# Kernel tuning notes

Measured on AMD Instinct MI355X. Metric: run time of the kernel, lower is better.

The kernel has to match this reference:

```python
import jax, jax.numpy as jnp
import numpy as np

WS = 8        # window_size
NH = 16       # num_heads

def setup_inputs() -> dict:
    key = jax.random.key(0)
    ks = jax.random.split(key, 6)
    B, H, W, C = 16, 64, 64, 512
    nW = (H // WS) * (W // WS)
    return {
        "x": jax.random.normal(ks[0], (B, H * W, C), jnp.float32),
        "qkv_w": jax.random.normal(ks[1], (3 * C, C), jnp.float32) * 0.02,
        "qkv_b": jax.random.normal(ks[2], (3 * C,), jnp.float32) * 0.02,
        "proj_w": jax.random.normal(ks[3], (C, C), jnp.float32) * 0.02,
        "proj_b": jax.random.normal(ks[4], (C,), jnp.float32) * 0.02,
        "attn_mask": jax.random.normal(ks[5], (nW, WS * WS, WS * WS), jnp.float32),
        "H": H,
        "W": W,
    }

def reference(x, qkv_w, qkv_b, proj_w, proj_b, attn_mask, H, W):
    B, N, C = x.shape
    ws = WS
    hd = C // NH
    scale = hd ** (-0.5)
    x_img = x.reshape(B, H, W, C)
    pad_h = (ws - H % ws) % ws
    pad_w = (ws - W % ws) % ws
    if pad_h > 0 or pad_w > 0:
        x_img = jnp.pad(x_img, ((0, 0), (0, pad_h), (0, pad_w), (0, 0)))
    Hp, Wp = H + pad_h, W + pad_w
    nW = (Hp // ws) * (Wp // ws)
    # window partition: [B*nW, ws*ws, C]
    x_win = x_img.reshape(B, Hp // ws, ws, Wp // ws, ws, C)
    x_win = x_win.transpose(0, 1, 3, 2, 4, 5).reshape(B * nW, ws * ws, C)
    # fused qkv projection (torch Linear: y = x @ W^T + b)
    qkv = x_win @ qkv_w.T + qkv_b
    qkv = qkv.reshape(B * nW, ws * ws, 3, NH, hd).transpose(2, 0, 3, 1, 4)
    q, k, v = qkv[0], qkv[1], qkv[2]  # each [B*nW, NH, ws*ws, hd]
    attn = jnp.einsum('bhqd,bhkd->bhqk', q, k) * scale
    if attn_mask is not None:
        attn = attn.reshape(B, nW, NH, ws * ws, ws * ws)
        attn = attn + attn_mask[None, :, None, :, :]
        attn = attn.reshape(B * nW, NH, ws * ws, ws * ws)
    attn = jax.nn.softmax(attn, axis=-1)
    out = jnp.einsum('bhqk,bhkd->bhqd', attn, v)
    out = out.transpose(0, 2, 1, 3).reshape(B * nW, ws * ws, C)
    out = out @ proj_w.T + proj_b
    # window reverse
    out = out.reshape(B, Hp // ws, Wp // ws, ws, ws, C)
    out = out.transpose(0, 1, 3, 2, 4, 5).reshape(B, Hp, Wp, C)
    out = out[:, :H, :W, :].reshape(B, H * W, C)
    return out
```

## Files before the change

kernel.cpp:

```cpp
#include <hip/hip_runtime.h>


typedef unsigned short u16;
typedef unsigned int u32;
typedef __attribute__((ext_vector_type(4))) u16 u16x4;
typedef __attribute__((ext_vector_type(8))) u16 u16x8;
typedef __attribute__((ext_vector_type(8))) short short8;
typedef __attribute__((ext_vector_type(4))) float f32x4;

__device__ __forceinline__ u16 f2bf(float f) {
    u32 u = __float_as_uint(f);
    u += 0x7fffu + ((u >> 16) & 1u);
    return (u16)(u >> 16);
}

__device__ __forceinline__ f32x4 MFMA(u16x8 a, u16x8 b, f32x4 c) {
    return __builtin_amdgcn_mfma_f32_16x16x32_bf16(
        __builtin_bit_cast(short8, a), __builtin_bit_cast(short8, b), c, 0, 0, 0);
}

__device__ __forceinline__ void gload16(const void* g, void* l) {
    __builtin_amdgcn_global_load_lds(
        (const __attribute__((address_space(1))) void*)g,
        (__attribute__((address_space(3))) void*)l, 16, 0, 0);
}

__device__ __forceinline__ int win2img(int r) {
    int b = r >> 12;
    int w = (r >> 6) & 63;
    int t = r & 63;
    int img = (((w >> 3) << 3) + (t >> 3)) * 64 + ((w & 7) << 3) + (t & 7);
    return (b << 12) + img;
}

__device__ __forceinline__ u16x8 cvt8(const float* src) {
    float4 a = *(const float4*)src;
    float4 b = *(const float4*)(src + 4);
    u16x8 t;
    t[0] = f2bf(a.x); t[1] = f2bf(a.y); t[2] = f2bf(a.z); t[3] = f2bf(a.w);
    t[4] = f2bf(b.x); t[5] = f2bf(b.y); t[6] = f2bf(b.z); t[7] = f2bf(b.w);
    return t;
}

__global__ __launch_bounds__(256)
void conv_f2b(const float* __restrict__ in, u16* __restrict__ out, int n8) {
    int u = blockIdx.x * 256 + threadIdx.x;
    if (u >= n8) return;
    *(u16x8*)(out + (size_t)u * 8) = cvt8(in + (size_t)u * 8);
}

__global__ __launch_bounds__(256)
void conv_permute_x(const float* __restrict__ x, u16* __restrict__ xw) {
    int u = blockIdx.x * 256 + threadIdx.x;
    int r = u >> 6;
    int c = (u & 63) << 3;
    int g = win2img(r);
    *(u16x8*)(xw + (size_t)r * 512 + c) = cvt8(x + (size_t)g * 512 + c);
}

__global__ __launch_bounds__(256)
void conv_maskT(const float* __restrict__ mask, float* __restrict__ mT) {
    __shared__ float t[64][65];
    const int w = blockIdx.x;
    const float* mp = mask + ((size_t)w << 12);
    float* op = mT + ((size_t)w << 12);
    const int r = threadIdx.x >> 2, c0 = (threadIdx.x & 3) << 4;
#pragma unroll
    for (int i = 0; i < 4; ++i) {
        float4 v = *(const float4*)(mp + (r << 6) + c0 + i * 4);
        t[c0 + i * 4 + 0][r] = v.x;
        t[c0 + i * 4 + 1][r] = v.y;
        t[c0 + i * 4 + 2][r] = v.z;
        t[c0 + i * 4 + 3][r] = v.w;
    }
    __syncthreads();
#pragma unroll
    for (int i = 0; i < 4; ++i) {
        float4 v;
        v.x = t[r][c0 + i * 4 + 0];
        v.y = t[r][c0 + i * 4 + 1];
        v.z = t[r][c0 + i * 4 + 2];
        v.w = t[r][c0 + i * 4 + 3];
        *(float4*)(op + (r << 6) + c0 + i * 4) = v;
    }
}

__global__ __launch_bounds__(256, 4)
void gemm_qkv(const u16* __restrict__ A, const u16* __restrict__ Wt,
              const float* __restrict__ bias, u16* __restrict__ QK,
              u16* __restrict__ VT)
{
    __shared__ char lds[32768];

    const int nwg = gridDim.x;
    const int q   = nwg >> 3;
    const int wg  = ((int)blockIdx.x & 7) * q + ((int)blockIdx.x >> 3);
    const int m0  = (wg / 12) * 128;
    const int n0  = (wg % 12) * 128;

    const int tid  = threadIdx.x;
    const int lane = tid & 63;
    const int wv   = tid >> 6;
    const int wm   = (wv >> 1) << 6;
    const int wn   = (wv & 1) << 6;
    const int lr   = lane & 15;
    const int lg   = lane >> 4;

    const char* aptr = (const char*)A + (((size_t)(m0 + (tid >> 2))) << 10) + ((tid & 3) << 4);
    const char* bptr = (const char*)Wt + (((size_t)(n0 + (tid >> 2))) << 10) + ((tid & 3) << 4);
    const u32 tb = (u32)tid << 4;

    f32x4 acc[4][4] = {};

#define STAGE(buf, kt) do {                                                   \
    const int ko_ = (kt) * 64;                                                \
    char* d_ = lds + (buf) * 16384 + tb;                                      \
    gload16(aptr + ko_,              d_);                                     \
    gload16(aptr + (64 << 10) + ko_, d_ + 4096);                              \
    gload16(bptr + ko_,              d_ + 8192);                              \
    gload16(bptr + (64 << 10) + ko_, d_ + 12288);                             \
} while (0)

#define COMPUTE(buf) do {                                                     \
    const u16* As_ = (const u16*)(lds + (buf) * 16384);                       \
    const u16* Bs_ = (const u16*)(lds + (buf) * 16384 + 8192);                \
    u16x8 af_[4], bf_[4];                                                     \
    _Pragma("unroll")                                                         \
    for (int mi = 0; mi < 4; ++mi)                                            \
        af_[mi] = *(const u16x8*)(As_ + (wm + mi * 16 + lr) * 32 + lg * 8);   \
    _Pragma("unroll")                                                         \
    for (int ni = 0; ni < 4; ++ni)                                            \
        bf_[ni] = *(const u16x8*)(Bs_ + (wn + ni * 16 + lr) * 32 + lg * 8);   \
    _Pragma("unroll")                                                         \
    for (int mi = 0; mi < 4; ++mi)                                            \
        _Pragma("unroll")                                                     \
        for (int ni = 0; ni < 4; ++ni)                                        \
            acc[mi][ni] = MFMA(af_[mi], bf_[ni], acc[mi][ni]);                \
} while (0)

    STAGE(0, 0);
    __syncthreads();

#pragma unroll 1
    for (int kt = 0; kt < 16; kt += 2) {
        STAGE(1, kt + 1);
        COMPUTE(0);
        __syncthreads();
        if (kt + 2 < 16) STAGE(0, kt + 2);
        COMPUTE(1);
        __syncthreads();
    }

    if (n0 < 1024) {
#pragma unroll
        for (int mi = 0; mi < 4; ++mi)
#pragma unroll
            for (int ni = 0; ni < 4; ++ni) {
                const int col = n0 + wn + ni * 16 + lr;
                const float bv = bias[col];
#pragma unroll
                for (int r = 0; r < 4; ++r) {
                    const int gr = m0 + wm + mi * 16 + lg * 4 + r;
                    QK[((size_t)gr << 10) + col] = f2bf(acc[mi][ni][r] + bv);
                }
            }
    } else {
#pragma unroll
        for (int mi = 0; mi < 4; ++mi) {
            const int gr0 = m0 + wm + mi * 16 + lg * 4;
            const int win = gr0 >> 6, ro = gr0 & 63;
#pragma unroll
            for (int ni = 0; ni < 4; ++ni) {
                const int col = n0 + wn + ni * 16 + lr;
                const float bv = bias[col];
                const int d = col - 1024;
                u16x4 h;
#pragma unroll
                for (int r = 0; r < 4; ++r) h[r] = f2bf(acc[mi][ni][r] + bv);
                *(u16x4*)(VT + (((size_t)win << 9) + d) * 64 + ro) = h;
            }
        }
    }
}

__global__ __launch_bounds__(256, 4)
void gemm_proj(const u16* __restrict__ A, const u16* __restrict__ Wt,
               const float* __restrict__ bias, float* __restrict__ C)
{
    __shared__ char lds[32768];

    const int nwg = gridDim.x;
    const int q   = nwg >> 3;
    const int wg  = ((int)blockIdx.x & 7) * q + ((int)blockIdx.x >> 3);
    const int m0  = (wg / 4) * 128;
    const int n0  = (wg % 4) * 128;

    const int tid  = threadIdx.x;
    const int lane = tid & 63;
    const int wv   = tid >> 6;
    const int wm   = (wv >> 1) << 6;
    const int wn   = (wv & 1) << 6;
    const int lr   = lane & 15;
    const int lg   = lane >> 4;

    const char* aptr = (const char*)A + (((size_t)(m0 + (tid >> 2))) << 10) + ((tid & 3) << 4);
    const char* bptr = (const char*)Wt + (((size_t)(n0 + (tid >> 2))) << 10) + ((tid & 3) << 4);
    const u32 tb = (u32)tid << 4;

    f32x4 acc[4][4] = {};

    STAGE(0, 0);
    __syncthreads();

#pragma unroll 1
    for (int kt = 0; kt < 16; kt += 2) {
        STAGE(1, kt + 1);
        COMPUTE(0);
        __syncthreads();
        if (kt + 2 < 16) STAGE(0, kt + 2);
        COMPUTE(1);
        __syncthreads();
    }

#undef STAGE
#undef COMPUTE

#pragma unroll
    for (int mi = 0; mi < 4; ++mi)
#pragma unroll
        for (int ni = 0; ni < 4; ++ni) {
            const int col = n0 + wn + ni * 16 + lr;
            const float bv = bias[col];
#pragma unroll
            for (int r = 0; r < 4; ++r) {
                const int gr = win2img(m0 + wm + mi * 16 + lg * 4 + r);
                C[((size_t)gr << 9) + col] = acc[mi][ni][r] + bv;
            }
        }
}

__global__ __launch_bounds__(256, 2)
void attn_kernel(const u16* __restrict__ QK, const u16* __restrict__ VT,
                 const float* __restrict__ mT, u16* __restrict__ attn_out)
{
    __shared__ __align__(16) u16 sP[4][64][72];

    const int tid  = threadIdx.x;
    const int lane = tid & 63;
    const int wv   = tid >> 6;
    const int lr   = lane & 15;
    const int lg   = lane >> 4;
    const int win  = blockIdx.x;
    const int wib  = win & 63;
    const size_t rb = (size_t)win << 6;
    const float* mtp = mT + ((size_t)wib << 12);
    const u16* vbase = VT + ((size_t)win << 15);
    const float scale = 0.17677669529663687f;

    u16x8 qf[2][4], kf[2][4], vf[2][2][2];

#define LOADH(hi_, b_) do {                                                   \
    const int hoff_ = ((hi_) * 4 + wv) * 32;                                  \
    _Pragma("unroll") for (int mt = 0; mt < 4; ++mt) {                        \
        const u16* rp_ = QK + ((rb + mt * 16 + lr) << 10) + hoff_ + lg * 8;   \
        qf[b_][mt] = *(const u16x8*)rp_;                                      \
        kf[b_][mt] = *(const u16x8*)(rp_ + 512);                              \
    }                                                                         \
    _Pragma("unroll") for (int k2_ = 0; k2_ < 2; ++k2_)                       \
    _Pragma("unroll") for (int nt_ = 0; nt_ < 2; ++nt_)                       \
        vf[b_][k2_][nt_] = *(const u16x8*)(vbase                              \
            + ((size_t)(hoff_ + nt_ * 16 + lr) << 6) + k2_ * 32 + lg * 8);    \
} while (0)

    LOADH(0, 0);

#pragma unroll
    for (int hi = 0; hi < 4; ++hi) {
        const int cb = hi & 1;
        const int hoff = (hi * 4 + wv) * 32;

        f32x4 s[4][4] = {};
#pragma unroll
        for (int mi = 0; mi < 4; ++mi)
#pragma unroll
            for (int ni = 0; ni < 4; ++ni)
                s[mi][ni] = MFMA(qf[cb][mi], kf[cb][ni], s[mi][ni]);

        if (hi < 3) LOADH(hi + 1, cb ^ 1);

        float rsum[4][4];
#pragma unroll
        for (int mi = 0; mi < 4; ++mi) {
            float4 mv[4];
#pragma unroll
            for (int ni = 0; ni < 4; ++ni)
                mv[ni] = *(const float4*)(mtp + (ni * 16 + lr) * 64 + mi * 16 + lg * 4);
#pragma unroll
            for (int r = 0; r < 4; ++r) {
                float vv[4];
                float mx = -1e30f;
#pragma unroll
                for (int ni = 0; ni < 4; ++ni) {
                    float v = s[mi][ni][r] * scale + ((const float*)&mv[ni])[r];
                    vv[ni] = v;
                    mx = fmaxf(mx, v);
                }
#pragma unroll
                for (int mk = 1; mk <= 8; mk <<= 1)
                    mx = fmaxf(mx, __shfl_xor(mx, mk, 64));
                float sum = 0.f;
#pragma unroll
                for (int ni = 0; ni < 4; ++ni) {
                    float p = __expf(vv[ni] - mx);
                    sum += p;
                    s[mi][ni][r] = p;
                }
#pragma unroll
                for (int mk = 1; mk <= 8; mk <<= 1)
                    sum += __shfl_xor(sum, mk, 64);
                rsum[mi][r] = sum;
            }
        }

        __syncthreads();
#pragma unroll
        for (int mi = 0; mi < 4; ++mi)
#pragma unroll
            for (int ni = 0; ni < 4; ++ni)
#pragma unroll
                for (int r = 0; r < 4; ++r)
                    sP[wv][mi * 16 + lg * 4 + r][ni * 16 + lr] = f2bf(s[mi][ni][r]);
        __syncthreads();

        u16x8 pf[4][2];
#pragma unroll
        for (int mt = 0; mt < 4; ++mt)
#pragma unroll
            for (int k2 = 0; k2 < 2; ++k2)
                pf[mt][k2] = *(const u16x8*)&sP[wv][mt * 16 + lr][k2 * 32 + lg * 8];

        f32x4 o[4][2] = {};
#pragma unroll
        for (int mt = 0; mt < 4; ++mt)
#pragma unroll
            for (int k2 = 0; k2 < 2; ++k2)
#pragma unroll
                for (int nt = 0; nt < 2; ++nt)
                    o[mt][nt] = MFMA(pf[mt][k2], vf[cb][k2][nt], o[mt][nt]);

#pragma unroll
        for (int mt = 0; mt < 4; ++mt)
#pragma unroll
            for (int nt = 0; nt < 2; ++nt)
#pragma unroll
                for (int r = 0; r < 4; ++r) {
                    const int row = mt * 16 + lg * 4 + r;
                    const int d = nt * 16 + lr;
                    attn_out[((rb + row) << 9) + hoff + d] =
                        f2bf(o[mt][nt][r] / rsum[mt][r]);
                }
    }
#undef LOADH
}

extern "C" void kernel_launch(void* const* d_in, const int* in_sizes, int n_in,
                              void* d_out, int out_size, void* d_ws, size_t ws_size,
                              hipStream_t stream)
{
    const float* x      = (const float*)d_in[0];
    const float* qkv_w  = (const float*)d_in[1];
    const float* qkv_b  = (const float*)d_in[2];
    const float* proj_w = (const float*)d_in[3];
    const float* proj_b = (const float*)d_in[4];
    const float* mask   = (const float*)d_in[5];
    float* out = (float*)d_out;

    const size_t WQKV  = 1536ull * 512;
    const size_t WPROJ = 512ull * 512;
    const size_t MTSZ  = 64ull * 64 * 64;

    u16* wq = (u16*)d_ws;
    u16* wp = wq + WQKV;
    float* mTg = (float*)(wp + WPROJ);
    u16* chunk = (u16*)(mTg + MTSZ);

    const size_t xwPB  = 4096ull * 512;
    const size_t qkPB  = 4096ull * 1024;
    const size_t vtPB  = 4096ull * 512;
    const size_t attPB = 4096ull * 512;
    const size_t perBatchBytes = (xwPB + qkPB + vtPB + attPB) * 2;

    size_t avail = ws_size - (WQKV + WPROJ) * 2 - MTSZ * 4;
    int Bc = (int)(avail / perBatchBytes);
    if (Bc > 16) Bc = 16;
    if (Bc < 1) Bc = 1;

    u16* xw_ws  = chunk;
    u16* qk_ws  = xw_ws + (size_t)Bc * xwPB;
    u16* vt_ws  = qk_ws + (size_t)Bc * qkPB;
    u16* att_ws = vt_ws + (size_t)Bc * vtPB;

    conv_f2b<<<dim3((WQKV / 8 + 255) / 256), 256, 0, stream>>>(qkv_w, wq, (int)(WQKV / 8));
    conv_f2b<<<dim3((WPROJ / 8 + 255) / 256), 256, 0, stream>>>(proj_w, wp, (int)(WPROJ / 8));
    conv_maskT<<<dim3(64), 256, 0, stream>>>(mask, mTg);

    for (int b0 = 0; b0 < 16; b0 += Bc) {
        const int bc = (16 - b0) < Bc ? (16 - b0) : Bc;
        const float* xc = x + (size_t)b0 * 4096 * 512;
        float* outc = out + (size_t)b0 * 4096 * 512;

        conv_permute_x<<<dim3(bc * 1024), 256, 0, stream>>>(xc, xw_ws);
        gemm_qkv<<<dim3(bc * 32 * 12), 256, 0, stream>>>(
            xw_ws, wq, qkv_b, qk_ws, vt_ws);
        attn_kernel<<<dim3(bc * 64), 256, 0, stream>>>(
            qk_ws, vt_ws, mTg, att_ws);
        gemm_proj<<<dim3(bc * 32 * 4), 256, 0, stream>>>(
            att_ws, wp, proj_b, outc);
    }
}
```

Measured before the change: 394.1 us.

## Store Q and K head-major per window and drop attention register double-buffering

The QKV GEMM epilogue now writes Q and K into separate head-major buffers ([window][head][64][32]), so each attention head's Q/K tile is one contiguous 4KB block and can be read without the 2KB row stride. The attention kernel drops its double-buffered Q/K/V register prefetch, loads each head just in time inside a non-unrolled loop, and raises the launch-bounds occupancy hint from 2 to 3. The aim is fewer scattered global reads and higher occupancy. The cost is less software prefetch overlap, and the epilogue writes become 2-byte scattered stores with a 64-byte stride.

```diff
diff --git a/kernel.cpp b/kernel.cpp
--- a/kernel.cpp
+++ b/kernel.cpp
@@ -84,33 +84,6 @@
         *(float4*)(op + (r << 6) + c0 + i * 4) = v;
     }
 }
-
-__global__ __launch_bounds__(256, 4)
-void gemm_qkv(const u16* __restrict__ A, const u16* __restrict__ Wt,
-              const float* __restrict__ bias, u16* __restrict__ QK,
-              u16* __restrict__ VT)
-{
-    __shared__ char lds[32768];
-
-    const int nwg = gridDim.x;
-    const int q   = nwg >> 3;
-    const int wg  = ((int)blockIdx.x & 7) * q + ((int)blockIdx.x >> 3);
-    const int m0  = (wg / 12) * 128;
-    const int n0  = (wg % 12) * 128;
-
-    const int tid  = threadIdx.x;
-    const int lane = tid & 63;
-    const int wv   = tid >> 6;
-    const int wm   = (wv >> 1) << 6;
-    const int wn   = (wv & 1) << 6;
-    const int lr   = lane & 15;
-    const int lg   = lane >> 4;
-
-    const char* aptr = (const char*)A + (((size_t)(m0 + (tid >> 2))) << 10) + ((tid & 3) << 4);
-    const char* bptr = (const char*)Wt + (((size_t)(n0 + (tid >> 2))) << 10) + ((tid & 3) << 4);
-    const u32 tb = (u32)tid << 4;
-
-    f32x4 acc[4][4] = {};
 
 #define STAGE(buf, kt) do {                                                   \
     const int ko_ = (kt) * 64;                                                \
@@ -138,62 +111,18 @@
             acc[mi][ni] = MFMA(af_[mi], bf_[ni], acc[mi][ni]);                \
 } while (0)
 
-    STAGE(0, 0);
-    __syncthreads();
-
-#pragma unroll 1
-    for (int kt = 0; kt < 16; kt += 2) {
-        STAGE(1, kt + 1);
-        COMPUTE(0);
-        __syncthreads();
-        if (kt + 2 < 16) STAGE(0, kt + 2);
-        COMPUTE(1);
-        __syncthreads();
-    }
-
-    if (n0 < 1024) {
-#pragma unroll
-        for (int mi = 0; mi < 4; ++mi)
-#pragma unroll
-            for (int ni = 0; ni < 4; ++ni) {
-                const int col = n0 + wn + ni * 16 + lr;
-                const float bv = bias[col];
-#pragma unroll
-                for (int r = 0; r < 4; ++r) {
-                    const int gr = m0 + wm + mi * 16 + lg * 4 + r;
-                    QK[((size_t)gr << 10) + col] = f2bf(acc[mi][ni][r] + bv);
-                }
-            }
-    } else {
-#pragma unroll
-        for (int mi = 0; mi < 4; ++mi) {
-            const int gr0 = m0 + wm + mi * 16 + lg * 4;
-            const int win = gr0 >> 6, ro = gr0 & 63;
-#pragma unroll
-            for (int ni = 0; ni < 4; ++ni) {
-                const int col = n0 + wn + ni * 16 + lr;
-                const float bv = bias[col];
-                const int d = col - 1024;
-                u16x4 h;
-#pragma unroll
-                for (int r = 0; r < 4; ++r) h[r] = f2bf(acc[mi][ni][r] + bv);
-                *(u16x4*)(VT + (((size_t)win << 9) + d) * 64 + ro) = h;
-            }
-        }
-    }
-}
-
 __global__ __launch_bounds__(256, 4)
-void gemm_proj(const u16* __restrict__ A, const u16* __restrict__ Wt,
-               const float* __restrict__ bias, float* __restrict__ C)
+void gemm_qkv(const u16* __restrict__ A, const u16* __restrict__ Wt,
+              const float* __restrict__ bias, u16* __restrict__ QH,
+              u16* __restrict__ KH, u16* __restrict__ VT)
 {
     __shared__ char lds[32768];
 
     const int nwg = gridDim.x;
     const int q   = nwg >> 3;
     const int wg  = ((int)blockIdx.x & 7) * q + ((int)blockIdx.x >> 3);
-    const int m0  = (wg / 4) * 128;
-    const int n0  = (wg % 4) * 128;
+    const int m0  = (wg / 12) * 128;
+    const int n0  = (wg % 12) * 128;
 
     const int tid  = threadIdx.x;
     const int lane = tid & 63;
@@ -222,8 +151,81 @@
         __syncthreads();
     }
 
-#undef STAGE
-#undef COMPUTE
+    if (n0 < 1024) {
+        u16* __restrict__ P = (n0 < 512) ? QH : KH;
+        const int cbase = (n0 < 512) ? n0 : (n0 - 512);
+#pragma unroll
+        for (int mi = 0; mi < 4; ++mi) {
+            const int gr0 = m0 + wm + mi * 16 + lg * 4;
+            const int win = gr0 >> 6, ro = gr0 & 63;
+#pragma unroll
+            for (int ni = 0; ni < 4; ++ni) {
+                const int col = cbase + wn + ni * 16 + lr;
+                const float bv = bias[(n0 < 512) ? col : (col + 512)];
+                const int h = col >> 5, c = col & 31;
+                u16* dst = P + (((size_t)win * 16 + h) << 11) + (ro << 5) + c;
+#pragma unroll
+                for (int r = 0; r < 4; ++r)
+                    dst[r << 5] = f2bf(acc[mi][ni][r] + bv);
+            }
+        }
+    } else {
+#pragma unroll
+        for (int mi = 0; mi < 4; ++mi) {
+            const int gr0 = m0 + wm + mi * 16 + lg * 4;
+            const int win = gr0 >> 6, ro = gr0 & 63;
+#pragma unroll
+            for (int ni = 0; ni < 4; ++ni) {
+                const int col = n0 + wn + ni * 16 + lr;
+                const float bv = bias[col];
+                const int d = col - 1024;
+                u16x4 h;
+#pragma unroll
+                for (int r = 0; r < 4; ++r) h[r] = f2bf(acc[mi][ni][r] + bv);
+                *(u16x4*)(VT + (((size_t)win << 9) + d) * 64 + ro) = h;
+            }
+        }
+    }
+}
+
+__global__ __launch_bounds__(256, 4)
+void gemm_proj(const u16* __restrict__ A, const u16* __restrict__ Wt,
+               const float* __restrict__ bias, float* __restrict__ C)
+{
+    __shared__ char lds[32768];
+
+    const int nwg = gridDim.x;
+    const int q   = nwg >> 3;
+    const int wg  = ((int)blockIdx.x & 7) * q + ((int)blockIdx.x >> 3);
+    const int m0  = (wg / 4) * 128;
+    const int n0  = (wg % 4) * 128;
+
+    const int tid  = threadIdx.x;
+    const int lane = tid & 63;
+    const int wv   = tid >> 6;
+    const int wm   = (wv >> 1) << 6;
+    const int wn   = (wv & 1) << 6;
+    const int lr   = lane & 15;
+    const int lg   = lane >> 4;
+
+    const char* aptr = (const char*)A + (((size_t)(m0 + (tid >> 2))) << 10) + ((tid & 3) << 4);
+    const char* bptr = (const char*)Wt + (((size_t)(n0 + (tid >> 2))) << 10) + ((tid & 3) << 4);
+    const u32 tb = (u32)tid << 4;
+
+    f32x4 acc[4][4] = {};
+
+    STAGE(0, 0);
+    __syncthreads();
+
+#pragma unroll 1
+    for (int kt = 0; kt < 16; kt += 2) {
+        STAGE(1, kt + 1);
+        COMPUTE(0);
+        __syncthreads();
+        if (kt + 2 < 16) STAGE(0, kt + 2);
+        COMPUTE(1);
+        __syncthreads();
+    }
 
 #pragma unroll
     for (int mi = 0; mi < 4; ++mi)
@@ -239,9 +241,13 @@
         }
 }
 
-__global__ __launch_bounds__(256, 2)
-void attn_kernel(const u16* __restrict__ QK, const u16* __restrict__ VT,
-                 const float* __restrict__ mT, u16* __restrict__ attn_out)
+#undef STAGE
+#undef COMPUTE
+
+__global__ __launch_bounds__(256, 3)
+void attn_kernel(const u16* __restrict__ QH, const u16* __restrict__ KH,
+                 const u16* __restrict__ VT, const float* __restrict__ mT,
+                 u16* __restrict__ attn_out)
 {
     __shared__ __align__(16) u16 sP[4][64][72];
 
@@ -254,39 +260,31 @@
     const int wib  = win & 63;
     const size_t rb = (size_t)win << 6;
     const float* mtp = mT + ((size_t)wib << 12);
+    const u16* qbase = QH + ((size_t)win << 15);
+    const u16* kbase = KH + ((size_t)win << 15);
     const u16* vbase = VT + ((size_t)win << 15);
     const float scale = 0.17677669529663687f;
 
-    u16x8 qf[2][4], kf[2][4], vf[2][2][2];
-
-#define LOADH(hi_, b_) do {                                                   \
-    const int hoff_ = ((hi_) * 4 + wv) * 32;                                  \
-    _Pragma("unroll") for (int mt = 0; mt < 4; ++mt) {                        \
-        const u16* rp_ = QK + ((rb + mt * 16 + lr) << 10) + hoff_ + lg * 8;   \
-        qf[b_][mt] = *(const u16x8*)rp_;                                      \
-        kf[b_][mt] = *(const u16x8*)(rp_ + 512);                              \
-    }                                                                         \
-    _Pragma("unroll") for (int k2_ = 0; k2_ < 2; ++k2_)                       \
-    _Pragma("unroll") for (int nt_ = 0; nt_ < 2; ++nt_)                       \
-        vf[b_][k2_][nt_] = *(const u16x8*)(vbase                              \
-            + ((size_t)(hoff_ + nt_ * 16 + lr) << 6) + k2_ * 32 + lg * 8);    \
-} while (0)
-
-    LOADH(0, 0);
-
-#pragma unroll
+#pragma unroll 1
     for (int hi = 0; hi < 4; ++hi) {
-        const int cb = hi & 1;
-        const int hoff = (hi * 4 + wv) * 32;
-
+        const int h = hi * 4 + wv;
+        const int hoff = h * 32;
+        const u16* qh = qbase + (h << 11);
+        const u16* kh = kbase + (h << 11);
+
+        u16x8 qf[4], kf[4];
+#pragma unroll
+        for (int mt = 0; mt < 4; ++mt) {
+            const int off = ((mt * 16 + lr) << 5) + (lg << 3);
+            qf[mt] = *(const u16x8*)(qh + off);
+            kf[mt] = *(const u16x8*)(kh + off);
+        }
         f32x4 s[4][4] = {};
 #pragma unroll
         for (int mi = 0; mi < 4; ++mi)
 #pragma unroll
             for (int ni = 0; ni < 4; ++ni)
-                s[mi][ni] = MFMA(qf[cb][mi], kf[cb][ni], s[mi][ni]);
-
-        if (hi < 3) LOADH(hi + 1, cb ^ 1);
+                s[mi][ni] = MFMA(qf[mi], kf[ni], s[mi][ni]);
 
         float rsum[4][4];
 #pragma unroll
@@ -339,6 +337,14 @@
             for (int k2 = 0; k2 < 2; ++k2)
                 pf[mt][k2] = *(const u16x8*)&sP[wv][mt * 16 + lr][k2 * 32 + lg * 8];
 
+        u16x8 vf[2][2];
+#pragma unroll
+        for (int k2 = 0; k2 < 2; ++k2)
+#pragma unroll
+            for (int nt = 0; nt < 2; ++nt)
+                vf[k2][nt] = *(const u16x8*)(vbase
+                    + ((size_t)(hoff + nt * 16 + lr) << 6) + k2 * 32 + lg * 8);
+
         f32x4 o[4][2] = {};
 #pragma unroll
         for (int mt = 0; mt < 4; ++mt)
@@ -346,7 +352,7 @@
             for (int k2 = 0; k2 < 2; ++k2)
 #pragma unroll
                 for (int nt = 0; nt < 2; ++nt)
-                    o[mt][nt] = MFMA(pf[mt][k2], vf[cb][k2][nt], o[mt][nt]);
+                    o[mt][nt] = MFMA(pf[mt][k2], vf[k2][nt], o[mt][nt]);
 
 #pragma unroll
         for (int mt = 0; mt < 4; ++mt)
@@ -360,7 +366,6 @@
                         f2bf(o[mt][nt][r] / rsum[mt][r]);
                 }
     }
-#undef LOADH
 }
 
 extern "C" void kernel_launch(void* const* d_in, const int* in_sizes, int n_in,
@@ -385,10 +390,11 @@
     u16* chunk = (u16*)(mTg + MTSZ);
 
     const size_t xwPB  = 4096ull * 512;
-    const size_t qkPB  = 4096ull * 1024;
+    const size_t qhPB  = 4096ull * 512;
+    const size_t khPB  = 4096ull * 512;
     const size_t vtPB  = 4096ull * 512;
     const size_t attPB = 4096ull * 512;
-    const size_t perBatchBytes = (xwPB + qkPB + vtPB + attPB) * 2;
+    const size_t perBatchBytes = (xwPB + qhPB + khPB + vtPB + attPB) * 2;
 
     size_t avail = ws_size - (WQKV + WPROJ) * 2 - MTSZ * 4;
     int Bc = (int)(avail / perBatchBytes);
@@ -396,8 +402,9 @@
     if (Bc < 1) Bc = 1;
 
     u16* xw_ws  = chunk;
-    u16* qk_ws  = xw_ws + (size_t)Bc * xwPB;
-    u16* vt_ws  = qk_ws + (size_t)Bc * qkPB;
+    u16* qh_ws  = xw_ws + (size_t)Bc * xwPB;
+    u16* kh_ws  = qh_ws + (size_t)Bc * qhPB;
+    u16* vt_ws  = kh_ws + (size_t)Bc * khPB;
     u16* att_ws = vt_ws + (size_t)Bc * vtPB;
 
     conv_f2b<<<dim3((WQKV / 8 + 255) / 256), 256, 0, stream>>>(qkv_w, wq, (int)(WQKV / 8));
@@ -411,9 +418,9 @@
 
         conv_permute_x<<<dim3(bc * 1024), 256, 0, stream>>>(xc, xw_ws);
         gemm_qkv<<<dim3(bc * 32 * 12), 256, 0, stream>>>(
-            xw_ws, wq, qkv_b, qk_ws, vt_ws);
+            xw_ws, wq, qkv_b, qh_ws, kh_ws, vt_ws);
         attn_kernel<<<dim3(bc * 64), 256, 0, stream>>>(
-            qk_ws, vt_ws, mTg, att_ws);
+            qh_ws, kh_ws, vt_ws, mTg, att_ws);
         gemm_proj<<<dim3(bc * 32 * 4), 256, 0, stream>>>(
             att_ws, wp, proj_b, outc);
     }
```

After: 338.9 us. -14.0%, faster.
